# Kernel optimization log

Hardware: AMD Instinct MI355X
Metric: run time of the kernel (lower is better)

## Reference

```python
import jax, jax.numpy as jnp
import numpy as np

O, I, B = 4096, 4096, 4096  # out_features, in_features, flattened tokens
GROUP = 128
INIT_PEAK = 2.0


def setup_inputs() -> dict:
    key = jax.random.key(0)
    k1, k2, k3, k4 = jax.random.split(key, 4)
    x = jax.random.normal(k1, (B, I), jnp.float32)
    # initial_ternary in {-1,0,1} -> theta init per the torch constructor
    tern = jax.random.randint(k2, (O, I), -1, 2)
    theta_neg = jnp.where(tern == -1, INIT_PEAK, -INIT_PEAK).astype(jnp.float32)
    theta_pos = jnp.where(tern == 1, INIT_PEAK, -INIT_PEAK).astype(jnp.float32)
    # per-group scales expanded to full weight shape (scales.unsqueeze(1).expand.reshape)
    n_groups = O * I // GROUP
    scales = jax.random.uniform(k3, (n_groups,), jnp.float32, 0.01, 0.05)
    scales_exp = jnp.repeat(scales, GROUP).reshape(O, I)
    # reparameterization noise (training path), made explicit for determinism
    eps = jax.random.normal(k4, (B, O), jnp.float32)
    return {"x": x, "theta_neg": theta_neg, "theta_pos": theta_pos,
            "scales_exp": scales_exp, "eps": eps}


def reference(x, theta_neg, theta_pos, scales_exp, eps):
    # stable 3-way softmax over logits [theta_neg, 0, theta_pos], done without
    # materializing the stacked [O, I, 3] tensor
    m = jnp.maximum(jnp.maximum(theta_neg, theta_pos), 0.0)
    e_neg = jnp.exp(theta_neg - m)
    e_zero = jnp.exp(-m)
    e_pos = jnp.exp(theta_pos - m)
    Z = e_neg + e_zero + e_pos
    p_neg = e_neg / Z
    p_pos = e_pos / Z
    diff = p_pos - p_neg
    w_mean = diff * scales_exp                                   # [O, I]
    w_var = (p_pos + p_neg - diff * diff) * (scales_exp * scales_exp)  # [O, I]
    mu = x @ w_mean.T                                            # [B, O]
    sigma_sq = (x * x) @ w_var.T                                 # [B, O]
    sigma = jnp.sqrt(jnp.maximum(sigma_sq, 1e-8))
    return mu + sigma * eps
```

## Files before the change

### kernel.cpp

```cpp
#include <hip/hip_runtime.h>

#define I_DIM 4096
#define O_DIM 4096
#define B_DIM 4096

typedef _Float16 f16;
typedef __attribute__((ext_vector_type(8))) _Float16 f16x8;
typedef __attribute__((ext_vector_type(4))) float f32x4;

struct f16pair { f16 m, v; };

__device__ inline f16pair lr_wmv(float tn, float tp, float s) {
    float m = fmaxf(fmaxf(tn, tp), 0.0f);
    float en = __expf(tn - m);
    float ez = __expf(-m);
    float ep = __expf(tp - m);
    float inv = __builtin_amdgcn_rcpf(en + ez + ep);
    float pn = en * inv, pp = ep * inv;
    float d = pp - pn;
    f16pair r;
    r.m = (f16)(d * s);
    r.v = (f16)((pp + pn - d * d) * (s * s));
    return r;
}

__global__ void prep_all(const float4* __restrict__ x, f16x8* __restrict__ xb8,
                         const float4* __restrict__ tn4, const float4* __restrict__ tp4,
                         const float4* __restrict__ sc4,
                         f16x8* __restrict__ wm8, f16x8* __restrict__ wv8,
                         int nbx) {
    const int bid = blockIdx.x;
    if (bid < nbx) {
        size_t i = (size_t)bid * blockDim.x + threadIdx.x;
        float4 a = x[2 * i];
        float4 b = x[2 * i + 1];
        f16x8 o;
        o[0] = (f16)a.x; o[1] = (f16)a.y; o[2] = (f16)a.z; o[3] = (f16)a.w;
        o[4] = (f16)b.x; o[5] = (f16)b.y; o[6] = (f16)b.z; o[7] = (f16)b.w;
        xb8[i] = o;
    } else {
        size_t i = (size_t)(bid - nbx) * blockDim.x + threadIdx.x;
        float4 a0 = tn4[2 * i], a1 = tn4[2 * i + 1];
        float4 b0 = tp4[2 * i], b1 = tp4[2 * i + 1];
        float4 s0 = sc4[2 * i], s1 = sc4[2 * i + 1];
        f16x8 om, ov;
        f16pair p;
        p = lr_wmv(a0.x, b0.x, s0.x); om[0] = p.m; ov[0] = p.v;
        p = lr_wmv(a0.y, b0.y, s0.y); om[1] = p.m; ov[1] = p.v;
        p = lr_wmv(a0.z, b0.z, s0.z); om[2] = p.m; ov[2] = p.v;
        p = lr_wmv(a0.w, b0.w, s0.w); om[3] = p.m; ov[3] = p.v;
        p = lr_wmv(a1.x, b1.x, s1.x); om[4] = p.m; ov[4] = p.v;
        p = lr_wmv(a1.y, b1.y, s1.y); om[5] = p.m; ov[5] = p.v;
        p = lr_wmv(a1.z, b1.z, s1.z); om[6] = p.m; ov[6] = p.v;
        p = lr_wmv(a1.w, b1.w, s1.w); om[7] = p.m; ov[7] = p.v;
        wm8[i] = om;
        wv8[i] = ov;
    }
}

#define BM 256
#define BN 128
#define BK 64

__device__ inline void gl_lds16(const f16* g, f16* l) {
    __builtin_amdgcn_global_load_lds(
        (const __attribute__((address_space(1))) unsigned int*)g,
        (__attribute__((address_space(3))) unsigned int*)l,
        16, 0, 0);
}

#define VM8 asm volatile("s_waitcnt vmcnt(8)")
#define VM6 asm volatile("s_waitcnt vmcnt(6)")
#define VM4 asm volatile("s_waitcnt vmcnt(4)")
#define VM0 asm volatile("s_waitcnt vmcnt(0)")
#define VMNONE (void)0

__global__ __launch_bounds__(512, 2)
void fused_dual_gemm(const f16* __restrict__ Xb,
                     const f16* __restrict__ Wm, const f16* __restrict__ Wv,
                     const float* __restrict__ eps, float* __restrict__ out) {
    __shared__ f16 smem[65536];

    const int tid  = threadIdx.x;
    const int lane = tid & 63;
    const int wave = tid >> 6;

    const int bm = blockIdx.y * BM;
    const int bn = blockIdx.x * BN;

    const int srow = lane >> 2;
    const int scol = (((lane & 3) ^ ((lane >> 3) & 3)) << 3);
    const f16* gX = Xb + (size_t)(bm + 32 * wave + srow) * I_DIM + scol;
    const f16* gM = Wm + (size_t)(bn + 16 * wave + srow) * I_DIM + scol;
    const f16* gV = Wv + (size_t)(bn + 16 * wave + srow) * I_DIM + scol;
    f16* ldsX = smem + wave * 1024;
    f16* ldsW = smem + 16384 + wave * 512;

    const int fr  = lane & 15;
    const int sg8 = (((lane >> 4) ^ ((fr >> 1) & 3)) << 3);
    const int m0 = (wave >> 1) << 6;
    const int n0 = (wave & 1) << 6;

    f32x4 accM[4][4];
    f32x4 accV[4][4];
    const f32x4 z = {0.0f, 0.0f, 0.0f, 0.0f};
#pragma unroll
    for (int mi = 0; mi < 4; ++mi)
#pragma unroll
        for (int ni = 0; ni < 4; ++ni) { accM[mi][ni] = z; accV[mi][ni] = z; }

    f16x8 a[4], a2[4];

#define STAGE_X(kelem, reg) do {                                               \
        gl_lds16(gX + (kelem),              ldsX + (reg));                     \
        gl_lds16(gX + (kelem) + 16 * I_DIM, ldsX + (reg) + 512);               \
    } while (0)
#define STAGE_W(kelem, reg) do {                                               \
        gl_lds16(gM + (kelem), ldsW + (reg));                                  \
        gl_lds16(gV + (kelem), ldsW + (reg) + 4096);                           \
    } while (0)

#define PHASE(RX, RW, NH, STG, VM) do {                                        \
        if ((NH) == 0) {                                                       \
            _Pragma("unroll")                                                  \
            for (int mi = 0; mi < 4; ++mi) {                                   \
                a[mi]  = *(const f16x8*)(smem + (RX) + (m0 + mi * 16 + fr) * 32 + sg8); \
                a2[mi] = a[mi] * a[mi];                                        \
            }                                                                  \
        }                                                                      \
        const f16x8 b0m = *(const f16x8*)(smem + (RW)        + (n0 + ((NH) * 2 + 0) * 16 + fr) * 32 + sg8); \
        const f16x8 b0v = *(const f16x8*)(smem + (RW) + 4096 + (n0 + ((NH) * 2 + 0) * 16 + fr) * 32 + sg8); \
        const f16x8 b1m = *(const f16x8*)(smem + (RW)        + (n0 + ((NH) * 2 + 1) * 16 + fr) * 32 + sg8); \
        const f16x8 b1v = *(const f16x8*)(smem + (RW) + 4096 + (n0 + ((NH) * 2 + 1) * 16 + fr) * 32 + sg8); \
        STG;                                                                   \
        __builtin_amdgcn_s_barrier();                                          \
        __builtin_amdgcn_s_setprio(1);                                         \
        _Pragma("unroll")                                                      \
        for (int mi = 0; mi < 4; ++mi) {                                       \
            accM[mi][(NH) * 2 + 0] = __builtin_amdgcn_mfma_f32_16x16x32_f16(a[mi],  b0m, accM[mi][(NH) * 2 + 0], 0, 0, 0); \
            accV[mi][(NH) * 2 + 0] = __builtin_amdgcn_mfma_f32_16x16x32_f16(a2[mi], b0v, accV[mi][(NH) * 2 + 0], 0, 0, 0); \
            accM[mi][(NH) * 2 + 1] = __builtin_amdgcn_mfma_f32_16x16x32_f16(a[mi],  b1m, accM[mi][(NH) * 2 + 1], 0, 0, 0); \
            accV[mi][(NH) * 2 + 1] = __builtin_amdgcn_mfma_f32_16x16x32_f16(a2[mi], b1v, accV[mi][(NH) * 2 + 1], 0, 0, 0); \
        }                                                                      \
        __builtin_amdgcn_s_setprio(0);                                         \
        VM;                                                                    \
        __builtin_amdgcn_s_barrier();                                          \
    } while (0)

    STAGE_X(0, 0);      STAGE_W(0, 0);
    STAGE_X(32, 8192);  STAGE_W(32, 8192);
    STAGE_X(64, 32768); STAGE_W(64, 32768);
    VM8;
    __builtin_amdgcn_s_barrier();

#pragma unroll 1
    for (int i = 0; i < 31; ++i) {
        const int kb = i * 128;
        PHASE(0,     16384, 0, STAGE_X(kb +  96, 40960), VMNONE);
        PHASE(0,     16384, 1, STAGE_W(kb +  96, 40960), VM6);
        PHASE(8192,  24576, 0, STAGE_X(kb + 128,     0), VMNONE);
        PHASE(8192,  24576, 1, STAGE_W(kb + 128,     0), VM6);
        PHASE(32768, 49152, 0, STAGE_X(kb + 160,  8192), VMNONE);
        PHASE(32768, 49152, 1, STAGE_W(kb + 160,  8192), VM6);
        PHASE(40960, 57344, 0, STAGE_X(kb + 192, 32768), VMNONE);
        PHASE(40960, 57344, 1, STAGE_W(kb + 192, 32768), VM6);
    }

    PHASE(0,     16384, 0, STAGE_X(4064, 40960), VMNONE);
    PHASE(0,     16384, 1, STAGE_W(4064, 40960), VM6);
    PHASE(8192,  24576, 0, VMNONE, VMNONE);
    PHASE(8192,  24576, 1, VMNONE, VM4);
    PHASE(32768, 49152, 0, VMNONE, VMNONE);
    PHASE(32768, 49152, 1, VMNONE, VM0);
    PHASE(40960, 57344, 0, VMNONE, VMNONE);
    PHASE(40960, 57344, 1, VMNONE, VMNONE);

    const int oc  = lane & 15;
    const int orb = (lane >> 4) << 2;
#pragma unroll
    for (int mi = 0; mi < 4; ++mi) {
#pragma unroll
        for (int ni = 0; ni < 4; ++ni) {
            const int gn = bn + n0 + ni * 16 + oc;
            const int gm = bm + m0 + mi * 16 + orb;
#pragma unroll
            for (int r = 0; r < 4; ++r) {
                const size_t off = (size_t)(gm + r) * O_DIM + gn;
                const float mu = accM[mi][ni][r];
                const float vv = accV[mi][ni][r];
                out[off] = fmaf(sqrtf(fmaxf(vv, 1e-8f)), eps[off], mu);
            }
        }
    }
#undef PHASE
#undef STAGE_X
#undef STAGE_W
}

extern "C" void kernel_launch(void* const* d_in, const int* in_sizes, int n_in,
                              void* d_out, int out_size, void* d_ws, size_t ws_size,
                              hipStream_t stream) {
    const float* x   = (const float*)d_in[0];
    const float* tn  = (const float*)d_in[1];
    const float* tp  = (const float*)d_in[2];
    const float* sc  = (const float*)d_in[3];
    const float* eps = (const float*)d_in[4];
    float* out = (float*)d_out;

    const size_t NE = (size_t)O_DIM * I_DIM;
    f16* xb = (f16*)d_ws;
    f16* wm = xb + NE;
    f16* wv = wm + NE;

    const int nbx = (int)(NE / 8 / 256);
    const int nbw = (int)(NE / 8 / 256);
    prep_all<<<nbx + nbw, 256, 0, stream>>>(
        (const float4*)x, (f16x8*)xb,
        (const float4*)tn, (const float4*)tp, (const float4*)sc,
        (f16x8*)wm, (f16x8*)wv, nbx);

    dim3 grid(O_DIM / BN, B_DIM / BM);
    fused_dual_gemm<<<grid, 512, 0, stream>>>(
        (const f16*)xb, (const f16*)wm, (const f16*)wv, eps, out);
}
```

Before: 545.0 us.

## Prefetch next LDS fragments into registers during MFMA phases

Restructures the GEMM main loop so LDS reads for the next phase's A and B fragments are issued after the current MFMA block, using double-buffered register sets (A0/A1, Ba/Bb). This removes the LDS-read latency that sat before each MFMA batch and halves the barriers per phase. In exchange it raises VGPR pressure, which may reduce occupancy, and the vmcnt wait points and buffer reuse timing shift, which adds hazard risk.

After: 535.5 us. About the same (-1.8%).

```diff
diff --git a/kernel.cpp b/kernel.cpp
--- a/kernel.cpp
+++ b/kernel.cpp
@@ -109,7 +109,7 @@
 #pragma unroll
         for (int ni = 0; ni < 4; ++ni) { accM[mi][ni] = z; accV[mi][ni] = z; }
 
-    f16x8 a[4], a2[4];
+    f16x8 A0[4], A1[4], A2c[4], Ba[4], Bb[4];
 
 #define STAGE_X(kelem, reg) do {                                               \
         gl_lds16(gX + (kelem),              ldsX + (reg));                     \
@@ -120,31 +120,43 @@
         gl_lds16(gV + (kelem), ldsW + (reg) + 4096);                           \
     } while (0)
 
-#define PHASE(RX, RW, NH, STG, VM) do {                                        \
-        if ((NH) == 0) {                                                       \
-            _Pragma("unroll")                                                  \
-            for (int mi = 0; mi < 4; ++mi) {                                   \
-                a[mi]  = *(const f16x8*)(smem + (RX) + (m0 + mi * 16 + fr) * 32 + sg8); \
-                a2[mi] = a[mi] * a[mi];                                        \
-            }                                                                  \
-        }                                                                      \
-        const f16x8 b0m = *(const f16x8*)(smem + (RW)        + (n0 + ((NH) * 2 + 0) * 16 + fr) * 32 + sg8); \
-        const f16x8 b0v = *(const f16x8*)(smem + (RW) + 4096 + (n0 + ((NH) * 2 + 0) * 16 + fr) * 32 + sg8); \
-        const f16x8 b1m = *(const f16x8*)(smem + (RW)        + (n0 + ((NH) * 2 + 1) * 16 + fr) * 32 + sg8); \
-        const f16x8 b1v = *(const f16x8*)(smem + (RW) + 4096 + (n0 + ((NH) * 2 + 1) * 16 + fr) * 32 + sg8); \
-        STG;                                                                   \
-        __builtin_amdgcn_s_barrier();                                          \
+#define RD_A(DST, RX) do {                                                     \
+        DST[0] = *(const f16x8*)(smem + (RX) + (m0 +  0 + fr) * 32 + sg8);     \
+        DST[1] = *(const f16x8*)(smem + (RX) + (m0 + 16 + fr) * 32 + sg8);     \
+        DST[2] = *(const f16x8*)(smem + (RX) + (m0 + 32 + fr) * 32 + sg8);     \
+        DST[3] = *(const f16x8*)(smem + (RX) + (m0 + 48 + fr) * 32 + sg8);     \
+    } while (0)
+#define RD_B(DST, RW, H) do {                                                  \
+        DST[0] = *(const f16x8*)(smem + (RW)        + (n0 + (H)*32 +  0 + fr) * 32 + sg8); \
+        DST[1] = *(const f16x8*)(smem + (RW) + 4096 + (n0 + (H)*32 +  0 + fr) * 32 + sg8); \
+        DST[2] = *(const f16x8*)(smem + (RW)        + (n0 + (H)*32 + 16 + fr) * 32 + sg8); \
+        DST[3] = *(const f16x8*)(smem + (RW) + 4096 + (n0 + (H)*32 + 16 + fr) * 32 + sg8); \
+    } while (0)
+
+#define MFMA16(AC, BB, NI0, NI1) do {                                          \
         __builtin_amdgcn_s_setprio(1);                                         \
         _Pragma("unroll")                                                      \
         for (int mi = 0; mi < 4; ++mi) {                                       \
-            accM[mi][(NH) * 2 + 0] = __builtin_amdgcn_mfma_f32_16x16x32_f16(a[mi],  b0m, accM[mi][(NH) * 2 + 0], 0, 0, 0); \
-            accV[mi][(NH) * 2 + 0] = __builtin_amdgcn_mfma_f32_16x16x32_f16(a2[mi], b0v, accV[mi][(NH) * 2 + 0], 0, 0, 0); \
-            accM[mi][(NH) * 2 + 1] = __builtin_amdgcn_mfma_f32_16x16x32_f16(a[mi],  b1m, accM[mi][(NH) * 2 + 1], 0, 0, 0); \
-            accV[mi][(NH) * 2 + 1] = __builtin_amdgcn_mfma_f32_16x16x32_f16(a2[mi], b1v, accV[mi][(NH) * 2 + 1], 0, 0, 0); \
+            accM[mi][NI0] = __builtin_amdgcn_mfma_f32_16x16x32_f16(AC[mi],  BB[0], accM[mi][NI0], 0, 0, 0); \
+            accV[mi][NI0] = __builtin_amdgcn_mfma_f32_16x16x32_f16(A2c[mi], BB[1], accV[mi][NI0], 0, 0, 0); \
+            accM[mi][NI1] = __builtin_amdgcn_mfma_f32_16x16x32_f16(AC[mi],  BB[2], accM[mi][NI1], 0, 0, 0); \
+            accV[mi][NI1] = __builtin_amdgcn_mfma_f32_16x16x32_f16(A2c[mi], BB[3], accV[mi][NI1], 0, 0, 0); \
         }                                                                      \
         __builtin_amdgcn_s_setprio(0);                                         \
-        VM;                                                                    \
-        __builtin_amdgcn_s_barrier();                                          \
+    } while (0)
+
+#define PH_EVEN(AC, RWcur, STG, VM) do {                                       \
+        _Pragma("unroll")                                                      \
+        for (int mi = 0; mi < 4; ++mi) A2c[mi] = AC[mi] * AC[mi];              \
+        MFMA16(AC, Ba, 0, 1);                                                  \
+        RD_B(Bb, RWcur, 1);                                                    \
+        STG; VM; __builtin_amdgcn_s_barrier();                                 \
+    } while (0)
+#define PH_ODD(AC, ANext, RXn, RWn, STG, VM) do {                              \
+        MFMA16(AC, Bb, 2, 3);                                                  \
+        RD_A(ANext, RXn);                                                      \
+        RD_B(Ba, RWn, 0);                                                      \
+        STG; VM; __builtin_amdgcn_s_barrier();                                 \
     } while (0)
 
     STAGE_X(0, 0);      STAGE_W(0, 0);
@@ -152,28 +164,30 @@
     STAGE_X(64, 32768); STAGE_W(64, 32768);
     VM8;
     __builtin_amdgcn_s_barrier();
+    RD_A(A0, 0);
+    RD_B(Ba, 16384, 0);
 
 #pragma unroll 1
     for (int i = 0; i < 31; ++i) {
         const int kb = i * 128;
-        PHASE(0,     16384, 0, STAGE_X(kb +  96, 40960), VMNONE);
-        PHASE(0,     16384, 1, STAGE_W(kb +  96, 40960), VM6);
-        PHASE(8192,  24576, 0, STAGE_X(kb + 128,     0), VMNONE);
-        PHASE(8192,  24576, 1, STAGE_W(kb + 128,     0), VM6);
-        PHASE(32768, 49152, 0, STAGE_X(kb + 160,  8192), VMNONE);
-        PHASE(32768, 49152, 1, STAGE_W(kb + 160,  8192), VM6);
-        PHASE(40960, 57344, 0, STAGE_X(kb + 192, 32768), VMNONE);
-        PHASE(40960, 57344, 1, STAGE_W(kb + 192, 32768), VM6);
+        PH_EVEN(A0, 16384,            STAGE_X(kb +  96, 40960), VM6);
+        PH_ODD (A0, A1, 8192, 24576,  STAGE_W(kb +  96, 40960), VMNONE);
+        PH_EVEN(A1, 24576,            STAGE_X(kb + 128,     0), VM6);
+        PH_ODD (A1, A0, 32768, 49152, STAGE_W(kb + 128,     0), VMNONE);
+        PH_EVEN(A0, 49152,            STAGE_X(kb + 160,  8192), VM6);
+        PH_ODD (A0, A1, 40960, 57344, STAGE_W(kb + 160,  8192), VMNONE);
+        PH_EVEN(A1, 57344,            STAGE_X(kb + 192, 32768), VM6);
+        PH_ODD (A1, A0, 0, 16384,     STAGE_W(kb + 192, 32768), VMNONE);
     }
 
-    PHASE(0,     16384, 0, STAGE_X(4064, 40960), VMNONE);
-    PHASE(0,     16384, 1, STAGE_W(4064, 40960), VM6);
-    PHASE(8192,  24576, 0, VMNONE, VMNONE);
-    PHASE(8192,  24576, 1, VMNONE, VM4);
-    PHASE(32768, 49152, 0, VMNONE, VMNONE);
-    PHASE(32768, 49152, 1, VMNONE, VM0);
-    PHASE(40960, 57344, 0, VMNONE, VMNONE);
-    PHASE(40960, 57344, 1, VMNONE, VMNONE);
+    PH_EVEN(A0, 16384,            STAGE_X(4064, 40960), VM6);
+    PH_ODD (A0, A1, 8192, 24576,  STAGE_W(4064, 40960), VMNONE);
+    PH_EVEN(A1, 24576,            VMNONE, VM4);
+    PH_ODD (A1, A0, 32768, 49152, VMNONE, VMNONE);
+    PH_EVEN(A0, 49152,            VMNONE, VM0);
+    PH_ODD (A0, A1, 40960, 57344, VMNONE, VMNONE);
+    PH_EVEN(A1, 57344,            VMNONE, VMNONE);
+    MFMA16(A1, Bb, 2, 3);
 
     const int oc  = lane & 15;
     const int orb = (lane >> 4) << 2;
@@ -192,9 +206,13 @@
             }
         }
     }
-#undef PHASE
+#undef PH_ODD
+#undef PH_EVEN
+#undef MFMA16
+#undef RD_B
+#undef RD_A
+#undef STAGE_W
 #undef STAGE_X
-#undef STAGE_W
 }
 
 extern "C" void kernel_launch(void* const* d_in, const int* in_sizes, int n_in,
```
